# Kernel optimization log

Hardware: AMD Instinct MI355X
Metric: run time of the kernel (lower is better)

## Reference

```python
import jax, jax.numpy as jnp
import numpy as np

D_MODEL = 1024
NHEAD = 16
HEAD_DIM = D_MODEL // NHEAD
MAX_LEN = 4096
ROPE_BASE = 500.0


def _rope_tables(L, dim):
    inv_freq = 1.0 / (ROPE_BASE ** (jnp.arange(0, dim, 2, dtype=jnp.float32) / dim))
    t = jnp.arange(L, dtype=jnp.float32)
    freqs = jnp.einsum('i,j->ij', t, inv_freq)  # [L, dim/2]
    emb = jnp.concatenate([freqs, freqs], axis=-1)  # [L, dim]
    return jnp.cos(emb), jnp.sin(emb)


def _rotate_half(x):
    x1, x2 = jnp.split(x, 2, axis=-1)
    return jnp.concatenate([-x2, x1], axis=-1)


def _apply_rope(x, cos, sin):
    return x * cos + _rotate_half(x) * sin


def setup_inputs() -> dict:
    key = jax.random.key(0)
    ks = jax.random.split(key, 6)
    B, L = 4, 2048
    bound_qkv = 1.0 / np.sqrt(D_MODEL)
    x = jax.random.normal(ks[0], (B, L, D_MODEL), dtype=jnp.float32)
    key_padding_mask = jnp.zeros((B, L), dtype=bool)
    W_qkv = jax.random.uniform(ks[1], (3 * D_MODEL, D_MODEL), jnp.float32, -bound_qkv, bound_qkv)
    b_qkv = jax.random.uniform(ks[2], (3 * D_MODEL,), jnp.float32, -bound_qkv, bound_qkv)
    W_out = jax.random.uniform(ks[3], (D_MODEL, D_MODEL), jnp.float32, -bound_qkv, bound_qkv)
    b_out = jax.random.uniform(ks[4], (D_MODEL,), jnp.float32, -bound_qkv, bound_qkv)
    return {"x": x, "key_padding_mask": key_padding_mask,
            "W_qkv": W_qkv, "b_qkv": b_qkv, "W_out": W_out, "b_out": b_out}


def reference(x, key_padding_mask, W_qkv, b_qkv, W_out, b_out):
    B, L, D = x.shape
    H, hd = NHEAD, HEAD_DIM
    qkv = x @ W_qkv.T + b_qkv  # [B, L, 3D]
    q, k, v = jnp.split(qkv, 3, axis=-1)
    # [B, H, L, hd]
    q = q.reshape(B, L, H, hd).transpose(0, 2, 1, 3)
    k = k.reshape(B, L, H, hd).transpose(0, 2, 1, 3)
    v = v.reshape(B, L, H, hd).transpose(0, 2, 1, 3)
    cos, sin = _rope_tables(L, hd)  # [L, hd]
    q = _apply_rope(q, cos, sin)
    k = _apply_rope(k, cos, sin)
    scores = jnp.einsum('bhqd,bhkd->bhqk', q, k) / jnp.sqrt(jnp.float32(hd))
    mask = key_padding_mask[:, None, None, :]  # [B,1,1,L]
    scores = jnp.where(mask, -jnp.inf, scores)
    attn = jax.nn.softmax(scores, axis=-1)
    out = jnp.einsum('bhqk,bhkd->bhqd', attn, v)
    out = out.transpose(0, 2, 1, 3).reshape(B, L, D)
    return out @ W_out.T + b_out
```

## Files before the change

### kernel.cpp

```cpp
#include <hip/hip_runtime.h>
#include <stdint.h>

typedef __attribute__((ext_vector_type(8))) __bf16 bf16x8;
typedef __attribute__((ext_vector_type(4))) short short4v;
typedef __attribute__((ext_vector_type(4))) float f32x4;

#if __has_builtin(__builtin_amdgcn_exp2f)
#define EXP2(x) __builtin_amdgcn_exp2f(x)
#else
#define EXP2(x) exp2f(x)
#endif

__device__ __forceinline__ short f2bf(float f) {
  union { float f; uint32_t u; } v; v.f = f;
  uint32_t r = (v.u + 0x7fffu + ((v.u >> 16) & 1u)) >> 16;
  return (short)(uint16_t)r;
}

__device__ __forceinline__ uint32_t pk2bf(float a, float b) {
  union { __bf16 h; uint16_t u; } x, y;
  x.h = (__bf16)a; y.h = (__bf16)b;
  return (uint32_t)x.u | ((uint32_t)y.u << 16);
}

__device__ __forceinline__ void gl2lds16(const void* g, const void* lds) {
  __builtin_amdgcn_global_load_lds(
      (const __attribute__((address_space(1))) void*)(uintptr_t)g,
      (__attribute__((address_space(3))) void*)(uint32_t)(uintptr_t)lds,
      16, 0, 0);
}

__device__ __forceinline__ bf16x8 frag8(const short* p) {
  return *(const bf16x8*)(const void*)p;
}

__global__ void convert3_k(const float* __restrict__ s0, short* __restrict__ d0, int n0,
                           const float* __restrict__ s1, short* __restrict__ d1, int n1,
                           const float* __restrict__ s2, short* __restrict__ d2, int n2) {
  int i = blockIdx.x * blockDim.x + threadIdx.x;
  int t0 = n0 >> 2, t1 = t0 + (n1 >> 2), t2 = t1 + (n2 >> 2);
  const float* s; short* d; int off;
  if (i < t0) { s = s0; d = d0; off = i; }
  else if (i < t1) { s = s1; d = d1; off = i - t0; }
  else if (i < t2) { s = s2; d = d2; off = i - t1; }
  else return;
  float4 v = ((const float4*)s)[off];
  short4v o;
  o.x = f2bf(v.x); o.y = f2bf(v.y); o.z = f2bf(v.z); o.w = f2bf(v.w);
  *(short4v*)(d + off * 4) = o;
}

__global__ void rope_tab_k(float* __restrict__ cosT, float* __restrict__ sinT,
                           const unsigned char* __restrict__ mask, float* __restrict__ maskf) {
  int i = blockIdx.x * blockDim.x + threadIdx.x;
  int pos = i >> 5, j = i & 31;
  float invf = exp2f(-(float)j * (8.965784284662087f / 32.0f));
  float ang = (float)pos * invf;
  float s, c;
  sincosf(ang, &s, &c);
  cosT[i] = c; sinT[i] = s;
  if (i < 8192) maskf[i] = mask[i] ? -1e30f : 0.0f;
}

template <int EPI>
__global__ __launch_bounds__(256, 3)
void gemm_bt_k(const short* __restrict__ A, const short* __restrict__ Bm,
               const float* __restrict__ bias, int N, int K,
               float* __restrict__ Cout,
               const float* __restrict__ cosT, const float* __restrict__ sinT,
               short* __restrict__ Qb, short* __restrict__ Kb, short* __restrict__ Vt) {
  __shared__ short As[2][128 * 32];
  __shared__ short Bs[2][128 * 32];
  const int tid = threadIdx.x;
  const int lane = tid & 63;
  const int w = tid >> 6;
  const int g = lane >> 4, l15 = lane & 15;
  const int wm = (w >> 1) * 64, wn = (w & 1) * 64;
  const int bm = blockIdx.x, bn = blockIdx.y;

  const int rseg = lane >> 2;
  const int cofs = ((lane & 3) ^ ((lane >> 3) & 3)) * 8;
  const int sA0 = w, sA1 = w + 4;
  const int arow0 = (bm * 128 + sA0 * 16 + rseg) * K;
  const int arow1 = (bm * 128 + sA1 * 16 + rseg) * K;
  const int brow0 = (bn * 128 + sA0 * 16 + rseg) * K;
  const int brow1 = (bn * 128 + sA1 * 16 + rseg) * K;

  const int rsw = (l15 >> 1) & 3;

  f32x4 acc[4][4];
#pragma unroll
  for (int i = 0; i < 4; i++)
#pragma unroll
    for (int j = 0; j < 4; j++) acc[i][j] = f32x4{0.f, 0.f, 0.f, 0.f};

  gl2lds16(A + arow0 + cofs, &As[0][sA0 * 512]);
  gl2lds16(A + arow1 + cofs, &As[0][sA1 * 512]);
  gl2lds16(Bm + brow0 + cofs, &Bs[0][sA0 * 512]);
  gl2lds16(Bm + brow1 + cofs, &Bs[0][sA1 * 512]);

  int cur = 0;
  for (int k0 = 0; k0 < K; k0 += 32, cur ^= 1) {
    __syncthreads();
    int nxt = cur ^ 1;
    int k1 = k0 + 32;
    if (k1 < K) {
      gl2lds16(A + arow0 + k1 + cofs, &As[nxt][sA0 * 512]);
      gl2lds16(A + arow1 + k1 + cofs, &As[nxt][sA1 * 512]);
      gl2lds16(Bm + brow0 + k1 + cofs, &Bs[nxt][sA0 * 512]);
      gl2lds16(Bm + brow1 + k1 + cofs, &Bs[nxt][sA1 * 512]);
    }
    bf16x8 af[4], bf[4];
#pragma unroll
    for (int im = 0; im < 4; im++) af[im] = frag8(&As[cur][(wm + im * 16 + l15) * 32 + (g ^ rsw) * 8]);
#pragma unroll
    for (int jn = 0; jn < 4; jn++) bf[jn] = frag8(&Bs[cur][(wn + jn * 16 + l15) * 32 + (g ^ rsw) * 8]);
#pragma unroll
    for (int im = 0; im < 4; im++)
#pragma unroll
      for (int jn = 0; jn < 4; jn++)
        acc[im][jn] = __builtin_amdgcn_mfma_f32_16x16x32_bf16(af[im], bf[jn], acc[im][jn], 0, 0, 0);
  }

  const int row0 = bm * 128 + wm + g * 4;
  const int col0 = bn * 128 + wn;

  if (EPI == 0) {
#pragma unroll
    for (int jn = 0; jn < 4; jn++) {
      float bb = bias[col0 + jn * 16 + l15];
#pragma unroll
      for (int im = 0; im < 4; im++)
#pragma unroll
        for (int r = 0; r < 4; r++) {
          int row = row0 + im * 16 + r;
          Cout[row * N + col0 + jn * 16 + l15] = acc[im][jn][r] + bb;
        }
    }
  } else {
#pragma unroll
    for (int jn = 0; jn < 4; jn++) {
      float bb = bias[col0 + jn * 16 + l15];
#pragma unroll
      for (int im = 0; im < 4; im++)
#pragma unroll
        for (int r = 0; r < 4; r++) acc[im][jn][r] += bb;
    }
    const int sector = col0 >> 10;
    const int h = (col0 & 1023) >> 6;
    if (sector == 2) {
#pragma unroll
      for (int jn = 0; jn < 4; jn++) {
        int d = jn * 16 + l15;
#pragma unroll
        for (int im = 0; im < 4; im++) {
          int row = row0 + im * 16;
          int b = row >> 11, pos = row & 2047;
          union { uint32_t u[2]; short4v s4; } pw;
          pw.u[0] = pk2bf(acc[im][jn][0], acc[im][jn][1]);
          pw.u[1] = pk2bf(acc[im][jn][2], acc[im][jn][3]);
          *(short4v*)&Vt[((b * 16 + h) * 64 + d) * 2048 + pos] = pw.s4;
        }
      }
    } else {
      short* dst = (sector == 0) ? Qb : Kb;
      const float scl = (sector == 0) ? 0.18033688011112042f : 1.0f;
#pragma unroll
      for (int jn = 0; jn < 4; jn++) {
        int d = jn * 16 + l15;
        int j = d & 31;
#pragma unroll
        for (int im = 0; im < 4; im++)
#pragma unroll
          for (int r = 0; r < 4; r++) {
            int row = row0 + im * 16 + r;
            int b = row >> 11, pos = row & 2047;
            float c = cosT[pos * 32 + j];
            float s = sinT[pos * 32 + j];
            float xv = acc[im][jn][r];
            float xp = acc[im][jn ^ 2][r];
            float rot = (jn < 2) ? -xp : xp;
            dst[((b * 16 + h) * 2048 + pos) * 64 + d] = f2bf((xv * c + rot * s) * scl);
          }
      }
    }
  }
}

__global__ __launch_bounds__(64, 2)
void attn_k(const short* __restrict__ Qb, const short* __restrict__ Kb,
            const short* __restrict__ Vt, const float* __restrict__ maskf,
            short* __restrict__ attn) {
  __shared__ short Ps[64 * 32];
  const int lane = threadIdx.x & 63;
  const int g = lane >> 4, l15 = lane & 15;
  const int fv = (l15 ^ (l15 >> 2)) & 3;
  const int bh = blockIdx.x, qw = blockIdx.y;
  const int b = bh >> 4, h = bh & 15;
  const int q0 = qw * 64;

  bf16x8 aq[4][2];
#pragma unroll
  for (int qi = 0; qi < 4; qi++)
#pragma unroll
    for (int kc = 0; kc < 2; kc++)
      aq[qi][kc] = frag8(Qb + (bh * 2048 + q0 + qi * 16 + l15) * 64 + kc * 32 + g * 8);

  bf16x8 aone;
#pragma unroll
  for (int i = 0; i < 8; i++) aone[i] = (__bf16)1.0f;

  f32x4 o[4][4];
#pragma unroll
  for (int jd = 0; jd < 4; jd++)
#pragma unroll
    for (int qi = 0; qi < 4; qi++) o[jd][qi] = f32x4{0.f, 0.f, 0.f, 0.f};
  f32x4 lacc[4];
#pragma unroll
  for (int qi = 0; qi < 4; qi++) lacc[qi] = f32x4{0.f, 0.f, 0.f, 0.f};

  const short* kp = Kb + (bh * 2048 + l15) * 64 + g * 8;
  const short* vp = Vt + (bh * 64 + l15) * 2048 + g * 8;
  const float* mp = maskf + b * 2048 + g * 4;

  bf16x8 kf[2][2], kn[2][2];
  f32x4 mf2[2], mn2[2];
#pragma unroll
  for (int kvt = 0; kvt < 2; kvt++) {
#pragma unroll
    for (int kc = 0; kc < 2; kc++) kf[kvt][kc] = frag8(kp + (kvt * 16) * 64 + kc * 32);
    mf2[kvt] = *(const f32x4*)(mp + kvt * 16);
  }

  for (int kt = 0; kt < 64; kt++) {
    const int kbase = kt * 32;
    if (kt + 1 < 64) {
      const int nb = kbase + 32;
#pragma unroll
      for (int kvt = 0; kvt < 2; kvt++) {
#pragma unroll
        for (int kc = 0; kc < 2; kc++) kn[kvt][kc] = frag8(kp + (nb + kvt * 16) * 64 + kc * 32);
        mn2[kvt] = *(const f32x4*)(mp + nb + kvt * 16);
      }
    }
    bf16x8 vf[4];
#pragma unroll
    for (int jd = 0; jd < 4; jd++)
      vf[jd] = frag8(vp + (jd * 16) * 2048 + kbase);

    f32x4 sv[4][2];
#pragma unroll
    for (int qi = 0; qi < 4; qi++)
#pragma unroll
      for (int kvt = 0; kvt < 2; kvt++) sv[qi][kvt] = mf2[kvt];
#pragma unroll
    for (int kvt = 0; kvt < 2; kvt++)
#pragma unroll
      for (int kc = 0; kc < 2; kc++)
#pragma unroll
        for (int qi = 0; qi < 4; qi++)
          sv[qi][kvt] = __builtin_amdgcn_mfma_f32_16x16x32_bf16(kf[kvt][kc], aq[qi][kc], sv[qi][kvt], 0, 0, 0);

#pragma unroll
    for (int qi = 0; qi < 4; qi++)
#pragma unroll
      for (int kvt = 0; kvt < 2; kvt++) {
        union { uint32_t u[2]; short4v s4; } pw;
        pw.u[0] = pk2bf(EXP2(sv[qi][kvt][0]), EXP2(sv[qi][kvt][1]));
        pw.u[1] = pk2bf(EXP2(sv[qi][kvt][2]), EXP2(sv[qi][kvt][3]));
        *(short4v*)&Ps[(qi * 16 + l15) * 32 + (((kvt * 2 + (g >> 1)) ^ fv) * 8) + (g & 1) * 4] = pw.s4;
      }

#pragma unroll
    for (int qi = 0; qi < 4; qi++) {
      bf16x8 bp = frag8(&Ps[(qi * 16 + l15) * 32 + (g ^ fv) * 8]);
#pragma unroll
      for (int jd = 0; jd < 4; jd++)
        o[jd][qi] = __builtin_amdgcn_mfma_f32_16x16x32_bf16(vf[jd], bp, o[jd][qi], 0, 0, 0);
      lacc[qi] = __builtin_amdgcn_mfma_f32_16x16x32_bf16(aone, bp, lacc[qi], 0, 0, 0);
    }

#pragma unroll
    for (int kvt = 0; kvt < 2; kvt++) {
#pragma unroll
      for (int kc = 0; kc < 2; kc++) kf[kvt][kc] = kn[kvt][kc];
      mf2[kvt] = mn2[kvt];
    }
  }

#pragma unroll
  for (int qi = 0; qi < 4; qi++) {
    float inv = 1.0f / lacc[qi][0];
    int q = q0 + qi * 16 + l15;
#pragma unroll
    for (int jd = 0; jd < 4; jd++) {
      union { uint32_t u[2]; short4v s4; } pw;
      pw.u[0] = pk2bf(o[jd][qi][0] * inv, o[jd][qi][1] * inv);
      pw.u[1] = pk2bf(o[jd][qi][2] * inv, o[jd][qi][3] * inv);
      *(short4v*)&attn[(b * 2048 + q) * 1024 + h * 64 + jd * 16 + g * 4] = pw.s4;
    }
  }
}

extern "C" void kernel_launch(void* const* d_in, const int* in_sizes, int n_in,
                              void* d_out, int out_size, void* d_ws, size_t ws_size,
                              hipStream_t stream) {
  const float* x = (const float*)d_in[0];
  const unsigned char* mask = (const unsigned char*)d_in[1];
  const float* W_qkv = (const float*)d_in[2];
  const float* b_qkv = (const float*)d_in[3];
  const float* W_out = (const float*)d_in[4];
  const float* b_out = (const float*)d_in[5];
  float* out = (float*)d_out;

  char* ws = (char*)d_ws;
  short* xb    = (short*)(ws + 0);
  short* wqkvb = (short*)(ws + 16777216);
  short* woutb = (short*)(ws + 23068672);
  float* cosT  = (float*)(ws + 25165824);
  float* sinT  = (float*)(ws + 25427968);
  short* Qb    = (short*)(ws + 25690112);
  short* Kb    = (short*)(ws + 42467328);
  short* Vtb   = (short*)(ws + 59244544);
  short* attnb = (short*)(ws + 76021760);
  float* maskf = (float*)(ws + 92798976);

  convert3_k<<<12288, 256, 0, stream>>>(x, xb, 8388608, W_qkv, wqkvb, 3145728, W_out, woutb, 1048576);
  rope_tab_k<<<256, 256, 0, stream>>>(cosT, sinT, mask, maskf);
  gemm_bt_k<1><<<dim3(64, 24), 256, 0, stream>>>(xb, wqkvb, b_qkv, 3072, 1024,
                                                 nullptr, cosT, sinT, Qb, Kb, Vtb);
  attn_k<<<dim3(64, 32), 64, 0, stream>>>(Qb, Kb, Vtb, maskf, attnb);
  gemm_bt_k<0><<<dim3(64, 8), 256, 0, stream>>>(attnb, woutb, b_out, 1024, 1024,
                                                out, nullptr, nullptr, nullptr, nullptr, nullptr);
}
```

Before: 321.9 us.

## Split attention KV range across two waves and combine partial results in LDS

The attention kernel now runs two wavefronts per block, and each wave processes half of the key/value sequence (1024 keys) for the same 64 queries. At the end, wave 1 writes its unnormalized output accumulators and row sums to shared memory, and wave 0 adds them in, normalizes and stores the result. The aim is to double the waves available to hide latency and shorten each wave's serial KV loop. The cost is extra LDS, two block barriers and a serial combine step. The combine relies on there being no running max, so the partial sums can simply be added.

```diff
diff --git a/kernel.cpp b/kernel.cpp
--- a/kernel.cpp
+++ b/kernel.cpp
@@ -187,17 +187,21 @@
   }
 }
 
-__global__ __launch_bounds__(64, 2)
+__global__ __launch_bounds__(128, 4)
 void attn_k(const short* __restrict__ Qb, const short* __restrict__ Kb,
             const short* __restrict__ Vt, const float* __restrict__ maskf,
             short* __restrict__ attn) {
-  __shared__ short Ps[64 * 32];
-  const int lane = threadIdx.x & 63;
+  __shared__ char smem[69 * 64 * 4];
+  const int tid = threadIdx.x;
+  const int lane = tid & 63, w = tid >> 6;
   const int g = lane >> 4, l15 = lane & 15;
   const int fv = (l15 ^ (l15 >> 2)) & 3;
   const int bh = blockIdx.x, qw = blockIdx.y;
   const int b = bh >> 4, h = bh & 15;
   const int q0 = qw * 64;
+  const int kw0 = w * 1024;
+
+  short* Ps = (short*)smem + w * 2048;
 
   bf16x8 aq[4][2];
 #pragma unroll
@@ -228,13 +232,13 @@
 #pragma unroll
   for (int kvt = 0; kvt < 2; kvt++) {
 #pragma unroll
-    for (int kc = 0; kc < 2; kc++) kf[kvt][kc] = frag8(kp + (kvt * 16) * 64 + kc * 32);
-    mf2[kvt] = *(const f32x4*)(mp + kvt * 16);
-  }
-
-  for (int kt = 0; kt < 64; kt++) {
-    const int kbase = kt * 32;
-    if (kt + 1 < 64) {
+    for (int kc = 0; kc < 2; kc++) kf[kvt][kc] = frag8(kp + (kw0 + kvt * 16) * 64 + kc * 32);
+    mf2[kvt] = *(const f32x4*)(mp + kw0 + kvt * 16);
+  }
+
+  for (int kt = 0; kt < 32; kt++) {
+    const int kbase = kw0 + kt * 32;
+    if (kt + 1 < 32) {
       const int nb = kbase + 32;
 #pragma unroll
       for (int kvt = 0; kvt < 2; kvt++) {
@@ -288,16 +292,31 @@
     }
   }
 
-#pragma unroll
-  for (int qi = 0; qi < 4; qi++) {
-    float inv = 1.0f / lacc[qi][0];
-    int q = q0 + qi * 16 + l15;
-#pragma unroll
-    for (int jd = 0; jd < 4; jd++) {
-      union { uint32_t u[2]; short4v s4; } pw;
-      pw.u[0] = pk2bf(o[jd][qi][0] * inv, o[jd][qi][1] * inv);
-      pw.u[1] = pk2bf(o[jd][qi][2] * inv, o[jd][qi][3] * inv);
-      *(short4v*)&attn[(b * 2048 + q) * 1024 + h * 64 + jd * 16 + g * 4] = pw.s4;
+  float* cb = (float*)smem;
+  __syncthreads();
+  if (w == 1) {
+#pragma unroll
+    for (int qi = 0; qi < 4; qi++) {
+#pragma unroll
+      for (int jd = 0; jd < 4; jd++)
+        *(f32x4*)&cb[lane * 69 + (qi * 4 + jd) * 4] = o[jd][qi];
+      cb[lane * 69 + 64 + qi] = lacc[qi][0];
+    }
+  }
+  __syncthreads();
+  if (w == 0) {
+#pragma unroll
+    for (int qi = 0; qi < 4; qi++) {
+      float inv = 1.0f / (lacc[qi][0] + cb[lane * 69 + 64 + qi]);
+      int q = q0 + qi * 16 + l15;
+#pragma unroll
+      for (int jd = 0; jd < 4; jd++) {
+        f32x4 t = o[jd][qi] + *(const f32x4*)&cb[lane * 69 + (qi * 4 + jd) * 4];
+        union { uint32_t u[2]; short4v s4; } pw;
+        pw.u[0] = pk2bf(t[0] * inv, t[1] * inv);
+        pw.u[1] = pk2bf(t[2] * inv, t[3] * inv);
+        *(short4v*)&attn[(b * 2048 + q) * 1024 + h * 64 + jd * 16 + g * 4] = pw.s4;
+      }
     }
   }
 }
@@ -329,7 +348,7 @@
   rope_tab_k<<<256, 256, 0, stream>>>(cosT, sinT, mask, maskf);
   gemm_bt_k<1><<<dim3(64, 24), 256, 0, stream>>>(xb, wqkvb, b_qkv, 3072, 1024,
                                                  nullptr, cosT, sinT, Qb, Kb, Vtb);
-  attn_k<<<dim3(64, 32), 64, 0, stream>>>(Qb, Kb, Vtb, maskf, attnb);
+  attn_k<<<dim3(64, 32), 128, 0, stream>>>(Qb, Kb, Vtb, maskf, attnb);
   gemm_bt_k<0><<<dim3(64, 8), 256, 0, stream>>>(attnb, woutb, b_out, 1024, 1024,
                                                 out, nullptr, nullptr, nullptr, nullptr, nullptr);
 }
```

Result: slower. 588.8 us (+82.9%).
